# Kernel optimization log

Measured on AMD Instinct MI355X. Metric: run time of the kernel, lower is better.

Reference implementation:

```python
import jax, jax.numpy as jnp
import numpy as np

STATE_DIM, ACTION_DIM, LATENT_DIM = 11, 3, 10
HID_VAE = (750, 750)
HID_Q = (400, 300)
N_SAMPLES = 10
PHI = 0.05
BATCH = 16384


def _linear_params(key, fan_in, fan_out):
    kw, kb = jax.random.split(key)
    lim = 1.0 / np.sqrt(fan_in)
    w = jax.random.uniform(kw, (fan_in, fan_out), minval=-lim, maxval=lim, dtype=jnp.float32)
    b = jax.random.uniform(kb, (fan_out,), minval=-lim, maxval=lim, dtype=jnp.float32)
    return w, b


def _mlp3(x, w1, b1, w2, b2, w3, b3):
    h = jax.nn.relu(x @ w1 + b1)
    h = jax.nn.relu(h @ w2 + b2)
    return h @ w3 + b3


def setup_inputs() -> dict:
    key = jax.random.key(0)
    ks = jax.random.split(key, 16)
    inp = {
        'states': jax.random.normal(ks[0], (BATCH, STATE_DIM), dtype=jnp.float32),
        'noise': jax.random.normal(ks[1], (BATCH * N_SAMPLES, LATENT_DIM), dtype=jnp.float32),
    }
    # VAE decoder: (state+latent) -> 750 -> 750 -> action, tanh
    inp['dec_w1'], inp['dec_b1'] = _linear_params(ks[2], STATE_DIM + LATENT_DIM, HID_VAE[1])
    inp['dec_w2'], inp['dec_b2'] = _linear_params(ks[3], HID_VAE[1], HID_VAE[0])
    inp['dec_w3'], inp['dec_b3'] = _linear_params(ks[4], HID_VAE[0], ACTION_DIM)
    # Actor_disturb: (state+action) -> 400 -> 300 -> action, tanh
    inp['act_w1'], inp['act_b1'] = _linear_params(ks[5], STATE_DIM + ACTION_DIM, HID_Q[0])
    inp['act_w2'], inp['act_b2'] = _linear_params(ks[6], HID_Q[0], HID_Q[1])
    inp['act_w3'], inp['act_b3'] = _linear_params(ks[7], HID_Q[1], ACTION_DIM)
    # Twin critics: (state+action) -> 400 -> 300 -> 1
    inp['q1_w1'], inp['q1_b1'] = _linear_params(ks[8], STATE_DIM + ACTION_DIM, HID_Q[0])
    inp['q1_w2'], inp['q1_b2'] = _linear_params(ks[9], HID_Q[0], HID_Q[1])
    inp['q1_w3'], inp['q1_b3'] = _linear_params(ks[10], HID_Q[1], 1)
    inp['q2_w1'], inp['q2_b1'] = _linear_params(ks[11], STATE_DIM + ACTION_DIM, HID_Q[0])
    inp['q2_w2'], inp['q2_b2'] = _linear_params(ks[12], HID_Q[0], HID_Q[1])
    inp['q2_w3'], inp['q2_b3'] = _linear_params(ks[13], HID_Q[1], 1)
    return inp


def reference(states, noise,
              dec_w1, dec_b1, dec_w2, dec_b2, dec_w3, dec_b3,
              act_w1, act_b1, act_w2, act_b2, act_w3, act_b3,
              q1_w1, q1_b1, q1_w2, q1_b2, q1_w3, q1_b3,
              q2_w1, q2_b1, q2_w2, q2_b2, q2_w3, q2_b3):
    bs = states.shape[0]
    # repeat_interleave(n_samples, 0)
    s = jnp.repeat(states, N_SAMPLES, axis=0)  # [bs*N, state_dim]
    # VAE.call_samples: clamped latent noise -> decoder -> tanh
    z = jnp.clip(noise, -0.5, 0.5)
    a = jnp.tanh(_mlp3(jnp.concatenate([s, z], axis=1),
                       dec_w1, dec_b1, dec_w2, dec_b2, dec_w3, dec_b3))
    # Actor_disturb: clamp(phi * tanh(mlp(s,a)) + a, -1, 1)
    da = jnp.tanh(_mlp3(jnp.concatenate([s, a], axis=1),
                        act_w1, act_b1, act_w2, act_b2, act_w3, act_b3))
    actions = jnp.clip(PHI * da + a, -1.0, 1.0)  # [bs*N, action_dim]
    # Twin Q values
    sa = jnp.concatenate([s, actions], axis=1)
    q1 = _mlp3(sa, q1_w1, q1_b1, q1_w2, q1_b2, q1_w3, q1_b3)
    q2 = _mlp3(sa, q2_w1, q2_b1, q2_w2, q2_b2, q2_w3, q2_b3)
    q = jnp.minimum(q1, q2).reshape(bs, N_SAMPLES)
    idx = jnp.argmax(q, axis=1)  # top-1 sample per state
    acts = actions.reshape(bs, N_SAMPLES, ACTION_DIM)
    ret = jnp.take_along_axis(acts, idx[:, None, None], axis=1)[:, 0, :]
    return ret
```

## Files before the change

kernel.cpp:

```cpp
#include <hip/hip_runtime.h>
#include <math.h>

typedef _Float16 f16;
typedef unsigned int u32;
typedef __attribute__((ext_vector_type(8))) _Float16 f16x8;
typedef __attribute__((ext_vector_type(16))) float f32x16;

#define LO_SCALE 4096.0f
#define LO_INV   2.44140625e-4f

__device__ __forceinline__ void split2f(float x, f16 &h, f16 &l) {
    h = (f16)x;
    l = (f16)((x - (float)h) * LO_SCALE);
}
__device__ __forceinline__ f32x16 mfma32(f16x8 a, f16x8 b, f32x16 c) {
    return __builtin_amdgcn_mfma_f32_32x32x16_f16(a, b, c, 0, 0, 0);
}

__global__ __launch_bounds__(256) void prep_frag(
    const float* __restrict__ W, int K, int N, int ksteps, int ntiles,
    f16* __restrict__ out)
{
    int total = ntiles * ksteps * 512;
    for (int i = blockIdx.x * blockDim.x + threadIdx.x; i < total;
         i += gridDim.x * blockDim.x) {
        int le = i & 511;
        int ks = (i >> 9) % ksteps;
        int nt = i / (512 * ksteps);
        int lane = le >> 3, e = le & 7;
        int n = nt * 32 + (lane & 31);
        int k = ks * 16 + (lane >> 5) * 8 + e;
        float w = (k < K && n < N) ? W[k * N + n] : 0.f;
        f16 h, l; split2f(w, h, l);
        size_t base = ((size_t)(nt * ksteps + ks) * 2) * 512 + le;
        out[base] = h;
        out[base + 512] = l;
    }
}

#define DEC_T 512
#define DEC_LDH 392

__global__ __launch_bounds__(512, 2) void dec_kernel(
    const float* __restrict__ states, const float* __restrict__ noise,
    const f16* __restrict__ w1f, const float* __restrict__ b1,
    const f16* __restrict__ w2f, const float* __restrict__ b2,
    const float* __restrict__ w3, const float* __restrict__ b3,
    float* __restrict__ adec)
{
    __shared__ float Xs[64][33];
    __shared__ __align__(16) f16 H1h[64 * DEC_LDH];
    __shared__ __align__(16) f16 H1l[64 * DEC_LDH];
    __shared__ float ow[8][64][3];

    const int tid = threadIdx.x;
    const int lane = tid & 63;
    const int wid = tid >> 6;
    const int l31 = lane & 31;
    const int l5  = lane >> 5;
    const int rowblk = blockIdx.x * 64;

    for (int idx = tid; idx < 64 * 32; idx += DEC_T) {
        int r = idx >> 5, c = idx & 31;
        int g = rowblk + r;
        float v = 0.f;
        if (c < 11) v = states[(g / 10) * 11 + c];
        else if (c < 21) {
            float z = noise[g * 10 + (c - 11)];
            v = fminf(fmaxf(z, -0.5f), 0.5f);
        }
        Xs[r][c] = v;
    }

    f32x16 am[3][2], ac[3][2];
    #pragma unroll
    for (int t = 0; t < 3; ++t)
        #pragma unroll
        for (int m = 0; m < 2; ++m)
            #pragma unroll
            for (int r = 0; r < 16; ++r) { am[t][m][r] = 0.f; ac[t][m][r] = 0.f; }

    __syncthreads();

    for (int h = 0; h < 2; ++h) {
        for (int rep = 0; rep < 2; ++rep) {
            if (rep == 1 && wid >= 4) break;
            int tl = (rep == 0) ? wid : 8 + wid;
            int nt = h * 12 + tl;
            #pragma unroll
            for (int m = 0; m < 2; ++m) {
                f32x16 pm, pc;
                #pragma unroll
                for (int r = 0; r < 16; ++r) { pm[r] = 0.f; pc[r] = 0.f; }
                #pragma unroll
                for (int ks = 0; ks < 2; ++ks) {
                    f16x8 xh, xl;
                    #pragma unroll
                    for (int e = 0; e < 8; ++e) {
                        float x = Xs[m * 32 + l31][ks * 16 + l5 * 8 + e];
                        f16 hh, ll; split2f(x, hh, ll);
                        xh[e] = hh; xl[e] = ll;
                    }
                    size_t base = ((size_t)(nt * 2 + ks) * 2) * 512 + lane * 8;
                    f16x8 bh = *(const f16x8*)&w1f[base];
                    f16x8 bl = *(const f16x8*)&w1f[base + 512];
                    pm = mfma32(xh, bh, pm);
                    pc = mfma32(xl, bh, pc);
                    pc = mfma32(xh, bl, pc);
                }
                int col = nt * 32 + l31;
                float bias = (col < 750) ? b1[col] : 0.f;
                int lc = tl * 32 + l31;
                #pragma unroll
                for (int r = 0; r < 16; ++r) {
                    int row = m * 32 + (r & 3) + 8 * (r >> 2) + 4 * l5;
                    float v = fmaxf(fmaf(pc[r], LO_INV, pm[r]) + bias, 0.f);
                    f16 hh, ll; split2f(v, hh, ll);
                    H1h[row * DEC_LDH + lc] = hh;
                    H1l[row * DEC_LDH + lc] = ll;
                }
            }
        }
        __syncthreads();

        for (int ks = 0; ks < 24; ++ks) {
            int ksg = h * 24 + ks;
            const f16x8 ah0 = *(const f16x8*)&H1h[l31 * DEC_LDH + ks * 16 + l5 * 8];
            const f16x8 al0 = *(const f16x8*)&H1l[l31 * DEC_LDH + ks * 16 + l5 * 8];
            const f16x8 ah1 = *(const f16x8*)&H1h[(32 + l31) * DEC_LDH + ks * 16 + l5 * 8];
            const f16x8 al1 = *(const f16x8*)&H1l[(32 + l31) * DEC_LDH + ks * 16 + l5 * 8];
            #pragma unroll
            for (int t = 0; t < 3; ++t) {
                int nt = wid + 8 * t;
                size_t base = ((size_t)(nt * 48 + ksg) * 2) * 512 + lane * 8;
                const f16x8 bh = *(const f16x8*)&w2f[base];
                const f16x8 bl = *(const f16x8*)&w2f[base + 512];
                am[t][0] = mfma32(ah0, bh, am[t][0]);
                ac[t][0] = mfma32(al0, bh, ac[t][0]);
                ac[t][0] = mfma32(ah0, bl, ac[t][0]);
                am[t][1] = mfma32(ah1, bh, am[t][1]);
                ac[t][1] = mfma32(al1, bh, ac[t][1]);
                ac[t][1] = mfma32(ah1, bl, ac[t][1]);
            }
        }
        __syncthreads();
    }

    #pragma unroll
    for (int t = 0; t < 3; ++t)
        #pragma unroll
        for (int m = 0; m < 2; ++m)
            #pragma unroll
            for (int r = 0; r < 16; ++r)
                am[t][m][r] = fmaf(ac[t][m][r], LO_INV, am[t][m][r]);

    #pragma unroll
    for (int j = 0; j < 3; ++j) {
        float p0[16], p1[16];
        #pragma unroll
        for (int r = 0; r < 16; ++r) { p0[r] = 0.f; p1[r] = 0.f; }
        #pragma unroll
        for (int t = 0; t < 3; ++t) {
            int col = (wid + 8 * t) * 32 + l31;
            float bias = 0.f, wv = 0.f;
            if (col < 750) { bias = b2[col]; wv = w3[col * 3 + j]; }
            #pragma unroll
            for (int r = 0; r < 16; ++r) {
                p0[r] += fmaxf(am[t][0][r] + bias, 0.f) * wv;
                p1[r] += fmaxf(am[t][1][r] + bias, 0.f) * wv;
            }
        }
        #pragma unroll
        for (int msk = 1; msk < 32; msk <<= 1) {
            #pragma unroll
            for (int r = 0; r < 16; ++r) {
                p0[r] += __shfl_xor(p0[r], msk);
                p1[r] += __shfl_xor(p1[r], msk);
            }
        }
        if (l31 == 0) {
            #pragma unroll
            for (int r = 0; r < 16; ++r) {
                int row = (r & 3) + 8 * (r >> 2) + 4 * l5;
                ow[wid][row][j] = p0[r];
                ow[wid][32 + row][j] = p1[r];
            }
        }
    }
    __syncthreads();
    if (tid < 192) {
        int row = tid / 3, j = tid - row * 3;
        float s = 0.f;
        #pragma unroll
        for (int w = 0; w < 8; ++w) s += ow[w][row][j];
        adec[(rowblk + row) * 3 + j] = tanhf(s + b3[j]);
    }
}

#define AQ_T 640
#define AQ_LDH 456

template<int NJ>
__device__ __forceinline__ void mlp_net2(
    const f16* __restrict__ w1f, const float* __restrict__ b1,
    const f16* __restrict__ w2f, const float* __restrict__ b2,
    const float* __restrict__ w3,
    const float (*Xs)[33], f16* H1h, f16* H1l, float (*ow)[64][3], int tid)
{
    const int lane = tid & 63;
    const int wid = tid >> 6;
    const int l31 = lane & 31;
    const int l5  = lane >> 5;

    for (int rep = 0; rep < 2; ++rep) {
        if (rep == 1 && wid >= 4) break;
        int t = (rep == 0) ? wid : 10 + wid;
        #pragma unroll
        for (int m = 0; m < 2; ++m) {
            f32x16 pm, pc;
            #pragma unroll
            for (int r = 0; r < 16; ++r) { pm[r] = 0.f; pc[r] = 0.f; }
            #pragma unroll
            for (int ks = 0; ks < 2; ++ks) {
                f16x8 xh, xl;
                #pragma unroll
                for (int e = 0; e < 8; ++e) {
                    float x = Xs[m * 32 + l31][ks * 16 + l5 * 8 + e];
                    f16 hh, ll; split2f(x, hh, ll);
                    xh[e] = hh; xl[e] = ll;
                }
                size_t base = ((size_t)(t * 2 + ks) * 2) * 512 + lane * 8;
                const f16x8 bh = *(const f16x8*)&w1f[base];
                const f16x8 bl = *(const f16x8*)&w1f[base + 512];
                pm = mfma32(xh, bh, pm);
                pc = mfma32(xl, bh, pc);
                pc = mfma32(xh, bl, pc);
            }
            int col = t * 32 + l31;
            float bias = (col < 400) ? b1[col] : 0.f;
            #pragma unroll
            for (int r = 0; r < 16; ++r) {
                int row = m * 32 + (r & 3) + 8 * (r >> 2) + 4 * l5;
                float v = fmaxf(fmaf(pc[r], LO_INV, pm[r]) + bias, 0.f);
                f16 hh, ll; split2f(v, hh, ll);
                H1h[row * AQ_LDH + col] = hh;
                H1l[row * AQ_LDH + col] = ll;
            }
        }
    }
    __syncthreads();

    f32x16 am0, ac0, am1, ac1;
    #pragma unroll
    for (int r = 0; r < 16; ++r) { am0[r] = 0.f; ac0[r] = 0.f; am1[r] = 0.f; ac1[r] = 0.f; }
    for (int ks = 0; ks < 28; ++ks) {
        const f16x8 ah0 = *(const f16x8*)&H1h[l31 * AQ_LDH + ks * 16 + l5 * 8];
        const f16x8 al0 = *(const f16x8*)&H1l[l31 * AQ_LDH + ks * 16 + l5 * 8];
        const f16x8 ah1 = *(const f16x8*)&H1h[(32 + l31) * AQ_LDH + ks * 16 + l5 * 8];
        const f16x8 al1 = *(const f16x8*)&H1l[(32 + l31) * AQ_LDH + ks * 16 + l5 * 8];
        size_t base = ((size_t)(wid * 28 + ks) * 2) * 512 + lane * 8;
        const f16x8 bh = *(const f16x8*)&w2f[base];
        const f16x8 bl = *(const f16x8*)&w2f[base + 512];
        am0 = mfma32(ah0, bh, am0);
        ac0 = mfma32(al0, bh, ac0);
        ac0 = mfma32(ah0, bl, ac0);
        am1 = mfma32(ah1, bh, am1);
        ac1 = mfma32(al1, bh, ac1);
        ac1 = mfma32(ah1, bl, ac1);
    }
    #pragma unroll
    for (int r = 0; r < 16; ++r) {
        am0[r] = fmaf(ac0[r], LO_INV, am0[r]);
        am1[r] = fmaf(ac1[r], LO_INV, am1[r]);
    }

    int col = wid * 32 + l31;
    #pragma unroll
    for (int j = 0; j < NJ; ++j) {
        float p0[16], p1[16];
        #pragma unroll
        for (int r = 0; r < 16; ++r) { p0[r] = 0.f; p1[r] = 0.f; }
        float bias = 0.f, wv = 0.f;
        if (col < 300) { bias = b2[col]; wv = w3[col * NJ + j]; }
        #pragma unroll
        for (int r = 0; r < 16; ++r) {
            p0[r] += fmaxf(am0[r] + bias, 0.f) * wv;
            p1[r] += fmaxf(am1[r] + bias, 0.f) * wv;
        }
        #pragma unroll
        for (int msk = 1; msk < 32; msk <<= 1) {
            #pragma unroll
            for (int r = 0; r < 16; ++r) {
                p0[r] += __shfl_xor(p0[r], msk);
                p1[r] += __shfl_xor(p1[r], msk);
            }
        }
        if (l31 == 0) {
            #pragma unroll
            for (int r = 0; r < 16; ++r) {
                int row = (r & 3) + 8 * (r >> 2) + 4 * l5;
                ow[wid][row][j] = p0[r];
                ow[wid][32 + row][j] = p1[r];
            }
        }
    }
}

__global__ __launch_bounds__(640, 3) void aq_kernel(
    const float* __restrict__ states, const float* __restrict__ adec,
    const f16* __restrict__ aw1f, const float* __restrict__ ab1,
    const f16* __restrict__ aw2f, const float* __restrict__ ab2,
    const float* __restrict__ aw3, const float* __restrict__ ab3,
    const f16* __restrict__ c1w1f, const float* __restrict__ c1b1,
    const f16* __restrict__ c1w2f, const float* __restrict__ c1b2,
    const float* __restrict__ c1w3, const float* __restrict__ c1b3,
    const f16* __restrict__ c2w1f, const float* __restrict__ c2b1,
    const f16* __restrict__ c2w2f, const float* __restrict__ c2b2,
    const float* __restrict__ c2w3, const float* __restrict__ c2b3,
    float* __restrict__ actions, float* __restrict__ qmin)
{
    __shared__ float Xs[64][33];
    __shared__ __align__(16) f16 H1h[64 * AQ_LDH];
    __shared__ __align__(16) f16 H1l[64 * AQ_LDH];
    __shared__ float ow[10][64][3];
    __shared__ float q1v[64];

    const int tid = threadIdx.x;
    const int rowblk = blockIdx.x * 64;

    for (int idx = tid; idx < 64 * 32; idx += AQ_T) {
        int r = idx >> 5, c = idx & 31;
        int g = rowblk + r;
        float v = 0.f;
        if (c < 11) v = states[(g / 10) * 11 + c];
        else if (c < 14) v = adec[g * 3 + (c - 11)];
        Xs[r][c] = v;
    }
    __syncthreads();

    mlp_net2<3>(aw1f, ab1, aw2f, ab2, aw3, Xs, H1h, H1l, ow, tid);
    __syncthreads();
    if (tid < 192) {
        int row = tid / 3, j = tid - row * 3;
        float s = 0.f;
        #pragma unroll
        for (int w = 0; w < 10; ++w) s += ow[w][row][j];
        float da = tanhf(s + ab3[j]);
        float ap = Xs[row][11 + j];
        float act = fminf(fmaxf(0.05f * da + ap, -1.f), 1.f);
        actions[(rowblk + row) * 3 + j] = act;
        Xs[row][11 + j] = act;
    }
    __syncthreads();

    mlp_net2<1>(c1w1f, c1b1, c1w2f, c1b2, c1w3, Xs, H1h, H1l, ow, tid);
    __syncthreads();
    if (tid < 64) {
        float s = 0.f;
        #pragma unroll
        for (int w = 0; w < 10; ++w) s += ow[w][tid][0];
        q1v[tid] = s + c1b3[0];
    }
    __syncthreads();

    mlp_net2<1>(c2w1f, c2b1, c2w2f, c2b2, c2w3, Xs, H1h, H1l, ow, tid);
    __syncthreads();
    if (tid < 64) {
        float s = 0.f;
        #pragma unroll
        for (int w = 0; w < 10; ++w) s += ow[w][tid][0];
        qmin[rowblk + tid] = fminf(q1v[tid], s + c2b3[0]);
    }
}

__global__ __launch_bounds__(256) void select_kernel(
    const float* __restrict__ qmin, const float* __restrict__ actions,
    float* __restrict__ out)
{
    int s = blockIdx.x * blockDim.x + threadIdx.x;
    if (s >= 16384) return;
    const float* q = qmin + s * 10;
    int best = 0;
    float bq = q[0];
    #pragma unroll
    for (int i = 1; i < 10; ++i) {
        float v = q[i];
        if (v > bq) { bq = v; best = i; }
    }
    const float* a = actions + (size_t)(s * 10 + best) * 3;
    out[s * 3 + 0] = a[0];
    out[s * 3 + 1] = a[1];
    out[s * 3 + 2] = a[2];
}

extern "C" void kernel_launch(void* const* d_in, const int* in_sizes, int n_in,
                              void* d_out, int out_size, void* d_ws, size_t ws_size,
                              hipStream_t stream)
{
    const float* states = (const float*)d_in[0];
    const float* noise  = (const float*)d_in[1];
    const float* dec_w1 = (const float*)d_in[2];
    const float* dec_b1 = (const float*)d_in[3];
    const float* dec_w2 = (const float*)d_in[4];
    const float* dec_b2 = (const float*)d_in[5];
    const float* dec_w3 = (const float*)d_in[6];
    const float* dec_b3 = (const float*)d_in[7];
    const float* act_w1 = (const float*)d_in[8];
    const float* act_b1 = (const float*)d_in[9];
    const float* act_w2 = (const float*)d_in[10];
    const float* act_b2 = (const float*)d_in[11];
    const float* act_w3 = (const float*)d_in[12];
    const float* act_b3 = (const float*)d_in[13];
    const float* q1_w1 = (const float*)d_in[14];
    const float* q1_b1 = (const float*)d_in[15];
    const float* q1_w2 = (const float*)d_in[16];
    const float* q1_b2 = (const float*)d_in[17];
    const float* q1_w3 = (const float*)d_in[18];
    const float* q1_b3 = (const float*)d_in[19];
    const float* q2_w1 = (const float*)d_in[20];
    const float* q2_b1 = (const float*)d_in[21];
    const float* q2_w2 = (const float*)d_in[22];
    const float* q2_b2 = (const float*)d_in[23];
    const float* q2_w3 = (const float*)d_in[24];
    const float* q2_b3 = (const float*)d_in[25];

    char* base = (char*)d_ws;
    size_t off = 0;
    auto carve = [&](size_t bytes) -> void* {
        void* p = base + off;
        off = (off + bytes + 255) & ~(size_t)255;
        return p;
    };
    f16* w1df = (f16*)carve((size_t)24 * 2 * 1024 * 2);
    f16* w2df = (f16*)carve((size_t)24 * 48 * 1024 * 2);
    f16* aw1f = (f16*)carve((size_t)14 * 2 * 1024 * 2);
    f16* aw2f = (f16*)carve((size_t)10 * 28 * 1024 * 2);
    f16* c1w1f = (f16*)carve((size_t)14 * 2 * 1024 * 2);
    f16* c1w2f = (f16*)carve((size_t)10 * 28 * 1024 * 2);
    f16* c2w1f = (f16*)carve((size_t)14 * 2 * 1024 * 2);
    f16* c2w2f = (f16*)carve((size_t)10 * 28 * 1024 * 2);
    float* adec = (float*)carve((size_t)163840 * 3 * 4);
    float* acts = (float*)carve((size_t)163840 * 3 * 4);
    float* qmn  = (float*)carve((size_t)163840 * 4);
    if (off > ws_size) return;

    auto prep = [&](const float* W, int K, int N, int ksteps, int ntiles, f16* out) {
        int total = ntiles * ksteps * 512;
        int grid = (total + 255) / 256;
        if (grid > 2048) grid = 2048;
        prep_frag<<<grid, 256, 0, stream>>>(W, K, N, ksteps, ntiles, out);
    };
    prep(dec_w1, 21, 750, 2, 24, w1df);
    prep(dec_w2, 750, 750, 48, 24, w2df);
    prep(act_w1, 14, 400, 2, 14, aw1f);
    prep(act_w2, 400, 300, 28, 10, aw2f);
    prep(q1_w1, 14, 400, 2, 14, c1w1f);
    prep(q1_w2, 400, 300, 28, 10, c1w2f);
    prep(q2_w1, 14, 400, 2, 14, c2w1f);
    prep(q2_w2, 400, 300, 28, 10, c2w2f);

    dec_kernel<<<2560, DEC_T, 0, stream>>>(states, noise,
        w1df, dec_b1, w2df, dec_b2, dec_w3, dec_b3, adec);

    aq_kernel<<<2560, AQ_T, 0, stream>>>(states, adec,
        aw1f, act_b1, aw2f, act_b2, act_w3, act_b3,
        c1w1f, q1_b1, c1w2f, q1_b2, q1_w3, q1_b3,
        c2w1f, q2_b1, c2w2f, q2_b2, q2_w3, q2_b3,
        acts, qmn);

    select_kernel<<<64, 256, 0, stream>>>(qmn, acts, (float*)d_out);
}
```

Before: 1.214 ms.

## Widen decoder to 12 waves and pre-split inputs to fp16 hi/lo in LDS

The decoder kernel goes from 8 to 12 waves per block. Each wave now owns one layer-1 tile and two contiguous layer-2 N-tiles instead of three strided ones, which removes the uneven second pass and lowers accumulator register pressure. Input rows are split once into fp16 hi/lo arrays in shared memory when loaded, so the MFMA loops read vectors directly instead of re-splitting floats per lane; the actor/critic kernel uses the same path. The trade-off is more threads per block, a larger ow buffer, and a small precision change, since the residual action is now rebuilt from the hi/lo halves.

```diff
diff --git a/kernel.cpp b/kernel.cpp
--- a/kernel.cpp
+++ b/kernel.cpp
@@ -38,20 +38,22 @@
     }
 }
 
-#define DEC_T 512
+#define DEC_T 768
 #define DEC_LDH 392
-
-__global__ __launch_bounds__(512, 2) void dec_kernel(
+#define XPITCH 40
+
+__global__ __launch_bounds__(768, 3) void dec_kernel(
     const float* __restrict__ states, const float* __restrict__ noise,
     const f16* __restrict__ w1f, const float* __restrict__ b1,
     const f16* __restrict__ w2f, const float* __restrict__ b2,
     const float* __restrict__ w3, const float* __restrict__ b3,
     float* __restrict__ adec)
 {
-    __shared__ float Xs[64][33];
+    __shared__ __align__(16) f16 Xh[64 * XPITCH];
+    __shared__ __align__(16) f16 Xl[64 * XPITCH];
     __shared__ __align__(16) f16 H1h[64 * DEC_LDH];
     __shared__ __align__(16) f16 H1l[64 * DEC_LDH];
-    __shared__ float ow[8][64][3];
+    __shared__ float ow[12][64][3];
 
     const int tid = threadIdx.x;
     const int lane = tid & 63;
@@ -69,12 +71,14 @@
             float z = noise[g * 10 + (c - 11)];
             v = fminf(fmaxf(z, -0.5f), 0.5f);
         }
-        Xs[r][c] = v;
-    }
-
-    f32x16 am[3][2], ac[3][2];
-    #pragma unroll
-    for (int t = 0; t < 3; ++t)
+        f16 hh, ll; split2f(v, hh, ll);
+        Xh[r * XPITCH + c] = hh;
+        Xl[r * XPITCH + c] = ll;
+    }
+
+    f32x16 am[2][2], ac[2][2];
+    #pragma unroll
+    for (int t = 0; t < 2; ++t)
         #pragma unroll
         for (int m = 0; m < 2; ++m)
             #pragma unroll
@@ -83,34 +87,36 @@
     __syncthreads();
 
     for (int h = 0; h < 2; ++h) {
-        for (int rep = 0; rep < 2; ++rep) {
-            if (rep == 1 && wid >= 4) break;
-            int tl = (rep == 0) ? wid : 8 + wid;
-            int nt = h * 12 + tl;
+        {
+            const int nt = h * 12 + wid;
+            const int col = nt * 32 + l31;
+            const float bias = (col < 750) ? b1[col] : 0.f;
             #pragma unroll
             for (int m = 0; m < 2; ++m) {
-                f32x16 pm, pc;
+                f32x16 pm;
                 #pragma unroll
-                for (int r = 0; r < 16; ++r) { pm[r] = 0.f; pc[r] = 0.f; }
+                for (int r = 0; r < 16; ++r) pm[r] = 0.f;
                 #pragma unroll
                 for (int ks = 0; ks < 2; ++ks) {
-                    f16x8 xh, xl;
-                    #pragma unroll
-                    for (int e = 0; e < 8; ++e) {
-                        float x = Xs[m * 32 + l31][ks * 16 + l5 * 8 + e];
-                        f16 hh, ll; split2f(x, hh, ll);
-                        xh[e] = hh; xl[e] = ll;
-                    }
+                    const f16x8 xh = *(const f16x8*)&Xh[(m * 32 + l31) * XPITCH + ks * 16 + l5 * 8];
                     size_t base = ((size_t)(nt * 2 + ks) * 2) * 512 + lane * 8;
-                    f16x8 bh = *(const f16x8*)&w1f[base];
-                    f16x8 bl = *(const f16x8*)&w1f[base + 512];
+                    const f16x8 bh = *(const f16x8*)&w1f[base];
                     pm = mfma32(xh, bh, pm);
+                }
+                f32x16 pc;
+                #pragma unroll
+                for (int r = 0; r < 16; ++r) pc[r] = 0.f;
+                #pragma unroll
+                for (int ks = 0; ks < 2; ++ks) {
+                    const f16x8 xh = *(const f16x8*)&Xh[(m * 32 + l31) * XPITCH + ks * 16 + l5 * 8];
+                    const f16x8 xl = *(const f16x8*)&Xl[(m * 32 + l31) * XPITCH + ks * 16 + l5 * 8];
+                    size_t base = ((size_t)(nt * 2 + ks) * 2) * 512 + lane * 8;
+                    const f16x8 bh = *(const f16x8*)&w1f[base];
+                    const f16x8 bl = *(const f16x8*)&w1f[base + 512];
                     pc = mfma32(xl, bh, pc);
                     pc = mfma32(xh, bl, pc);
                 }
-                int col = nt * 32 + l31;
-                float bias = (col < 750) ? b1[col] : 0.f;
-                int lc = tl * 32 + l31;
+                const int lc = wid * 32 + l31;
                 #pragma unroll
                 for (int r = 0; r < 16; ++r) {
                     int row = m * 32 + (r & 3) + 8 * (r >> 2) + 4 * l5;
@@ -124,14 +130,14 @@
         __syncthreads();
 
         for (int ks = 0; ks < 24; ++ks) {
-            int ksg = h * 24 + ks;
+            const int ksg = h * 24 + ks;
             const f16x8 ah0 = *(const f16x8*)&H1h[l31 * DEC_LDH + ks * 16 + l5 * 8];
             const f16x8 al0 = *(const f16x8*)&H1l[l31 * DEC_LDH + ks * 16 + l5 * 8];
             const f16x8 ah1 = *(const f16x8*)&H1h[(32 + l31) * DEC_LDH + ks * 16 + l5 * 8];
             const f16x8 al1 = *(const f16x8*)&H1l[(32 + l31) * DEC_LDH + ks * 16 + l5 * 8];
             #pragma unroll
-            for (int t = 0; t < 3; ++t) {
-                int nt = wid + 8 * t;
+            for (int t = 0; t < 2; ++t) {
+                const int nt = wid * 2 + t;
                 size_t base = ((size_t)(nt * 48 + ksg) * 2) * 512 + lane * 8;
                 const f16x8 bh = *(const f16x8*)&w2f[base];
                 const f16x8 bl = *(const f16x8*)&w2f[base + 512];
@@ -147,7 +153,7 @@
     }
 
     #pragma unroll
-    for (int t = 0; t < 3; ++t)
+    for (int t = 0; t < 2; ++t)
         #pragma unroll
         for (int m = 0; m < 2; ++m)
             #pragma unroll
@@ -160,8 +166,8 @@
         #pragma unroll
         for (int r = 0; r < 16; ++r) { p0[r] = 0.f; p1[r] = 0.f; }
         #pragma unroll
-        for (int t = 0; t < 3; ++t) {
-            int col = (wid + 8 * t) * 32 + l31;
+        for (int t = 0; t < 2; ++t) {
+            int col = (wid * 2 + t) * 32 + l31;
             float bias = 0.f, wv = 0.f;
             if (col < 750) { bias = b2[col]; wv = w3[col * 3 + j]; }
             #pragma unroll
@@ -192,7 +198,7 @@
         int row = tid / 3, j = tid - row * 3;
         float s = 0.f;
         #pragma unroll
-        for (int w = 0; w < 8; ++w) s += ow[w][row][j];
+        for (int w = 0; w < 12; ++w) s += ow[w][row][j];
         adec[(rowblk + row) * 3 + j] = tanhf(s + b3[j]);
     }
 }
@@ -205,7 +211,7 @@
     const f16* __restrict__ w1f, const float* __restrict__ b1,
     const f16* __restrict__ w2f, const float* __restrict__ b2,
     const float* __restrict__ w3,
-    const float (*Xs)[33], f16* H1h, f16* H1l, float (*ow)[64][3], int tid)
+    const f16* Xh, const f16* Xl, f16* H1h, f16* H1l, float (*ow)[64][3], int tid)
 {
     const int lane = tid & 63;
     const int wid = tid >> 6;
@@ -222,13 +228,8 @@
             for (int r = 0; r < 16; ++r) { pm[r] = 0.f; pc[r] = 0.f; }
             #pragma unroll
             for (int ks = 0; ks < 2; ++ks) {
-                f16x8 xh, xl;
-                #pragma unroll
-                for (int e = 0; e < 8; ++e) {
-                    float x = Xs[m * 32 + l31][ks * 16 + l5 * 8 + e];
-                    f16 hh, ll; split2f(x, hh, ll);
-                    xh[e] = hh; xl[e] = ll;
-                }
+                const f16x8 xh = *(const f16x8*)&Xh[(m * 32 + l31) * XPITCH + ks * 16 + l5 * 8];
+                const f16x8 xl = *(const f16x8*)&Xl[(m * 32 + l31) * XPITCH + ks * 16 + l5 * 8];
                 size_t base = ((size_t)(t * 2 + ks) * 2) * 512 + lane * 8;
                 const f16x8 bh = *(const f16x8*)&w1f[base];
                 const f16x8 bl = *(const f16x8*)&w1f[base + 512];
@@ -319,7 +320,8 @@
     const float* __restrict__ c2w3, const float* __restrict__ c2b3,
     float* __restrict__ actions, float* __restrict__ qmin)
 {
-    __shared__ float Xs[64][33];
+    __shared__ __align__(16) f16 Xh[64 * XPITCH];
+    __shared__ __align__(16) f16 Xl[64 * XPITCH];
     __shared__ __align__(16) f16 H1h[64 * AQ_LDH];
     __shared__ __align__(16) f16 H1l[64 * AQ_LDH];
     __shared__ float ow[10][64][3];
@@ -334,11 +336,13 @@
         float v = 0.f;
         if (c < 11) v = states[(g / 10) * 11 + c];
         else if (c < 14) v = adec[g * 3 + (c - 11)];
-        Xs[r][c] = v;
-    }
-    __syncthreads();
-
-    mlp_net2<3>(aw1f, ab1, aw2f, ab2, aw3, Xs, H1h, H1l, ow, tid);
+        f16 hh, ll; split2f(v, hh, ll);
+        Xh[r * XPITCH + c] = hh;
+        Xl[r * XPITCH + c] = ll;
+    }
+    __syncthreads();
+
+    mlp_net2<3>(aw1f, ab1, aw2f, ab2, aw3, Xh, Xl, H1h, H1l, ow, tid);
     __syncthreads();
     if (tid < 192) {
         int row = tid / 3, j = tid - row * 3;
@@ -346,14 +350,17 @@
         #pragma unroll
         for (int w = 0; w < 10; ++w) s += ow[w][row][j];
         float da = tanhf(s + ab3[j]);
-        float ap = Xs[row][11 + j];
+        float ap = (float)Xh[row * XPITCH + 11 + j]
+                 + (float)Xl[row * XPITCH + 11 + j] * LO_INV;
         float act = fminf(fmaxf(0.05f * da + ap, -1.f), 1.f);
         actions[(rowblk + row) * 3 + j] = act;
-        Xs[row][11 + j] = act;
-    }
-    __syncthreads();
-
-    mlp_net2<1>(c1w1f, c1b1, c1w2f, c1b2, c1w3, Xs, H1h, H1l, ow, tid);
+        f16 hh, ll; split2f(act, hh, ll);
+        Xh[row * XPITCH + 11 + j] = hh;
+        Xl[row * XPITCH + 11 + j] = ll;
+    }
+    __syncthreads();
+
+    mlp_net2<1>(c1w1f, c1b1, c1w2f, c1b2, c1w3, Xh, Xl, H1h, H1l, ow, tid);
     __syncthreads();
     if (tid < 64) {
         float s = 0.f;
@@ -363,7 +370,7 @@
     }
     __syncthreads();
 
-    mlp_net2<1>(c2w1f, c2b1, c2w2f, c2b2, c2w3, Xs, H1h, H1l, ow, tid);
+    mlp_net2<1>(c2w1f, c2b1, c2w2f, c2b2, c2w3, Xh, Xl, H1h, H1l, ow, tid);
     __syncthreads();
     if (tid < 64) {
         float s = 0.f;
```

After: 1.862 ms. 1.53x slower.
